# Performance work log

Measured on AMD Instinct MI355X. Metric: run time of the kernel, lower is better.

Reference implementation:

```python
import jax, jax.numpy as jnp
import numpy as np
from jax import lax

WS = 7          # window size
SHIFT = WS // 2 # shift for odd blocks
NH = 4          # num heads
PATCH = 4


def _rel_index(ws):
    # standard Swin relative position index, shape (ws*ws, ws*ws)
    coords = np.stack(np.meshgrid(np.arange(ws), np.arange(ws), indexing='ij')).reshape(2, -1)
    rel = (coords[:, :, None] - coords[:, None, :]).transpose(1, 2, 0)
    rel[..., 0] += ws - 1
    rel[..., 1] += ws - 1
    rel[..., 0] *= 2 * ws - 1
    return jnp.asarray(rel.sum(-1))


def _attn_mask(H, W, ws, s):
    # BasicLayer mask for cyclic shift: (nW, ws*ws, ws*ws) with 0 / -100
    img = np.zeros((H, W))
    cnt = 0
    for hs in (slice(0, -ws), slice(-ws, -s), slice(-s, None)):
        for wsl in (slice(0, -ws), slice(-ws, -s), slice(-s, None)):
            img[hs, wsl] = cnt
            cnt += 1
    mw = img.reshape(H // ws, ws, W // ws, ws).transpose(0, 2, 1, 3).reshape(-1, ws * ws)
    diff = mw[:, None, :] - mw[:, :, None]
    return jnp.asarray(np.where(diff != 0, -100.0, 0.0).astype(np.float32))


def setup_inputs() -> dict:
    key = jax.random.key(0)
    ks = jax.random.split(key, 6)
    C = 128
    return {
        'x': jax.random.normal(ks[0], (16, 3, 448, 448), jnp.float32),
        'conv_w': jax.random.normal(ks[1], (C, 3, PATCH, PATCH), jnp.float32) * 0.02,
        'conv_b': jnp.zeros((C,), jnp.float32),
        'qkv_w': jax.random.normal(ks[2], (2, 3 * C, C), jnp.float32) * 0.02,
        'qkv_b': jnp.zeros((2, 3 * C), jnp.float32),
        'proj_w': jax.random.normal(ks[3], (2, C, C), jnp.float32) * 0.02,
        'proj_b': jnp.zeros((2, C), jnp.float32),
        'rpb': jax.random.normal(ks[4], (2, (2 * WS - 1) ** 2, NH), jnp.float32) * 0.02,
    }


def _forward(x, conv_w, conv_b, qkv_w, qkv_b, proj_w, proj_b, rpb):
    # patch embed: strided conv
    y = lax.conv_general_dilated(x, conv_w, (PATCH, PATCH), 'VALID',
                                 dimension_numbers=('NCHW', 'OIHW', 'NCHW'))
    y = y + conv_b[None, :, None, None]
    B, C, H, W = y.shape
    hd = C // NH
    scale = hd ** -0.5
    N = WS * WS
    nW = (H // WS) * (W // WS)
    t = y.reshape(B, C, H * W).transpose(0, 2, 1)  # (B, L, C)

    rel_idx = _rel_index(WS)                    # (N, N)
    mask = _attn_mask(H, W, WS, SHIFT)          # (nW, N, N)

    for i in range(2):
        shift = 0 if i % 2 == 0 else SHIFT
        xw = t.reshape(B, H, W, C)
        if shift > 0:
            xw = jnp.roll(xw, (-shift, -shift), axis=(1, 2))
        # window partition -> (B*nW, N, C)
        win = xw.reshape(B, H // WS, WS, W // WS, WS, C).transpose(0, 1, 3, 2, 4, 5).reshape(-1, N, C)
        qkv = win @ qkv_w[i].T + qkv_b[i]       # (B*nW, N, 3C)
        qkv = qkv.reshape(-1, N, 3, NH, hd).transpose(2, 0, 3, 1, 4)
        q, k, v = qkv[0], qkv[1], qkv[2]        # (B*nW, NH, N, hd)
        attn = jnp.einsum('wnid,wnjd->wnij', q * scale, k)
        bias = rpb[i][rel_idx].transpose(2, 0, 1)  # (NH, N, N)
        attn = attn + bias[None]
        if shift > 0:
            attn = (attn.reshape(B, nW, NH, N, N) + mask[None, :, None]).reshape(-1, NH, N, N)
        attn = jax.nn.softmax(attn, axis=-1)
        out = jnp.einsum('wnij,wnjd->wnid', attn, v).transpose(0, 2, 1, 3).reshape(-1, N, C)
        out = out @ proj_w[i].T + proj_b[i]
        # window reverse
        xw = out.reshape(B, H // WS, W // WS, WS, WS, C).transpose(0, 1, 3, 2, 4, 5).reshape(B, H, W, C)
        if shift > 0:
            xw = jnp.roll(xw, (shift, shift), axis=(1, 2))
        t = xw.reshape(B, H * W, C)

    return t.reshape(B, H, W, C).transpose(0, 3, 1, 2)  # (B, C, H, W)


def reference(x, conv_w, conv_b, qkv_w, qkv_b, proj_w, proj_b, rpb):
    return _forward(x, conv_w, conv_b, qkv_w, qkv_b, proj_w, proj_b, rpb)
```

## Files before the change

### kernel.cpp

```cpp
#include <hip/hip_runtime.h>

#define BB 16
#define CC 128
#define HH 112
#define NHH 4
#define WSZ 7
#define NN 49
#define SH 3

typedef _Float16 h8 __attribute__((ext_vector_type(8)));
typedef _Float16 h4 __attribute__((ext_vector_type(4)));
typedef float f4 __attribute__((ext_vector_type(4)));

__device__ __forceinline__ int rid3(int p) { return p < 105 ? 0 : (p < 109 ? 1 : 2); }

#define SWZ(row, j, CH) ((row) * ((CH) * 8) + (((((j) >> 3) ^ (row)) & ((CH) - 1)) << 3) + ((j) & 7))

__device__ __forceinline__ h4 pack4(f4 v) {
  h4 r; r[0] = (_Float16)v[0]; r[1] = (_Float16)v[1];
  r[2] = (_Float16)v[2]; r[3] = (_Float16)v[3];
  return r;
}

__global__ __launch_bounds__(256) void conv_embed(const float* __restrict__ x,
    const float* __restrict__ cw, const float* __restrict__ cb, _Float16* __restrict__ t0) {
  __shared__ float xs[3][4][448];
  __shared__ float wT[48][128];
  __shared__ float cbs[128];
  int bid = blockIdx.x;
  int b = bid / HH, oh = bid % HH;
  int tid = threadIdx.x;
  for (int idx = tid; idx < 3 * 4 * 448; idx += 256) {
    int ch = idx / 1792;
    int r = (idx / 448) & 3;
    int col = idx % 448;
    xs[ch][r][col] = x[((b * 3 + ch) * 448 + (oh * 4 + r)) * 448 + col];
  }
  for (int idx = tid; idx < 6144; idx += 256) {
    int c = idx / 48, k = idx - c * 48;
    wT[k][c] = cw[idx];
  }
  if (tid < 128) cbs[tid] = cb[tid];
  __syncthreads();
  int c0 = (tid & 31) << 2;
  int gg = tid >> 5;
  for (int it = 0; it < 4; ++it) {
    int gw0 = it * 32 + gg * 4;
    if (gw0 >= HH) break;
    float acc[4][4] = {};
#pragma unroll
    for (int k = 0; k < 48; ++k) {
      int ch = k >> 4, r = (k >> 2) & 3, j = k & 3;
      float4 wv = *(const float4*)&wT[k][c0];
#pragma unroll
      for (int d = 0; d < 4; ++d) {
        float xv = xs[ch][r][(gw0 + d) * 4 + j];
        acc[d][0] = fmaf(xv, wv.x, acc[d][0]);
        acc[d][1] = fmaf(xv, wv.y, acc[d][1]);
        acc[d][2] = fmaf(xv, wv.z, acc[d][2]);
        acc[d][3] = fmaf(xv, wv.w, acc[d][3]);
      }
    }
    float4 bv = *(const float4*)&cbs[c0];
#pragma unroll
    for (int d = 0; d < 4; ++d) {
      int gw = gw0 + d;
      h4 o;
      o[0] = (_Float16)(acc[d][0] + bv.x); o[1] = (_Float16)(acc[d][1] + bv.y);
      o[2] = (_Float16)(acc[d][2] + bv.z); o[3] = (_Float16)(acc[d][3] + bv.w);
      *(h4*)&t0[((size_t)(b * HH + oh) * HH + gw) * CC + c0] = o;
    }
  }
}

__global__ void prep(const float* __restrict__ qw, const float* __restrict__ qb,
                     const float* __restrict__ pw, const float* __restrict__ rpb,
                     _Float16* __restrict__ qwh, float* __restrict__ qbs,
                     _Float16* __restrict__ pwh, _Float16* __restrict__ biasT) {
  const float scale = 0.17677669529663687f;
  int tid0 = blockIdx.x * blockDim.x + threadIdx.x;
  int stride = gridDim.x * blockDim.x;
  for (int idx = tid0; idx < 2 * 384 * 128; idx += stride) {
    int n = (idx >> 7) % 384;
    float v = qw[idx];
    if (n < 128) v *= scale;
    qwh[idx] = (_Float16)v;
  }
  for (int idx = tid0; idx < 2 * 384; idx += stride) {
    int n = idx % 384;
    float v = qb[idx];
    if (n < 128) v *= scale;
    qbs[idx] = v;
  }
  for (int idx = tid0; idx < 2 * 128 * 128; idx += stride)
    pwh[idx] = (_Float16)pw[idx];
  for (int idx = tid0; idx < 2 * 4 * 4 * 4 * 64 * 4; idx += stride) {
    int r = idx & 3;
    int lane = (idx >> 2) & 63;
    int it = (idx >> 8) & 3;
    int jt = (idx >> 10) & 3;
    int hh = (idx >> 12) & 3;
    int ll = idx >> 14;
    int i = it * 16 + (lane & 15);
    int j = jt * 16 + ((lane >> 4) * 4) + r;
    float v = 0.f;
    if (i < NN && j < NN) {
      int rel = ((i / 7 - j / 7) + 6) * 13 + ((i % 7 - j % 7) + 6);
      v = rpb[(ll * 169 + rel) * NHH + hh];
    }
    biasT[idx] = (_Float16)v;
  }
}

#define RA 0
#define RB 8192
__global__ __launch_bounds__(256, 4) void swin_layer(
    const _Float16* __restrict__ tin, _Float16* __restrict__ toutB, float* __restrict__ outN,
    const _Float16* __restrict__ qwh, const float* __restrict__ qbs,
    const _Float16* __restrict__ pwh, const float* __restrict__ pb,
    const _Float16* __restrict__ biasT, int shift, int writeN) {
  __shared__ _Float16 sm[16384];

  int tid = threadIdx.x;
  int wid = (blockIdx.x & 7) * 512 + (blockIdx.x >> 3);
  int b = wid >> 8;
  int wh = (wid >> 4) & 15, ww = wid & 15;
  int w = tid >> 6, l = tid & 63, li = l & 15, lg = l >> 4;
  int h = w;
  const int hb = RB + h * 2048;

  for (int c = tid; c < 64 * 16; c += 256) {
    int n = c >> 4, k0 = (c & 15) * 8;
    int gh = wh * WSZ + n / 7 + shift; if (gh >= HH) gh -= HH;
    int gw = ww * WSZ + n % 7 + shift; if (gw >= HH) gw -= HH;
    h8 v = *(const h8*)(tin + ((size_t)(b * HH + gh) * HH + gw) * CC + k0);
    *(h8*)&sm[RA + SWZ(n, k0, 16)] = v;
  }
  __syncthreads();

  h8 Kf[4], Qf[4];

  {
    f4 accK[2][4], accQ[2][4];
#pragma unroll
    for (int half = 0; half < 2; ++half) {
      float4 bk = *(const float4*)&qbs[128 + h * 32 + half * 16 + lg * 4];
      float4 bq = *(const float4*)&qbs[h * 32 + half * 16 + lg * 4];
#pragma unroll
      for (int nt = 0; nt < 4; ++nt) {
        accK[half][nt] = f4{bk.x, bk.y, bk.z, bk.w};
        accQ[half][nt] = f4{bq.x, bq.y, bq.z, bq.w};
      }
    }
#pragma unroll
    for (int ks = 0; ks < 4; ++ks) {
      h8 bW[4];
#pragma unroll
      for (int nt = 0; nt < 4; ++nt)
        bW[nt] = *(const h8*)&sm[RA + SWZ(nt * 16 + li, ks * 32 + lg * 8, 16)];
#pragma unroll
      for (int half = 0; half < 2; ++half) {
        h8 aK = *(const h8*)(qwh + (size_t)((8 + 2 * h + half) * 16 + li) * 128 + ks * 32 + lg * 8);
        h8 aQ = *(const h8*)(qwh + (size_t)((2 * h + half) * 16 + li) * 128 + ks * 32 + lg * 8);
#pragma unroll
        for (int nt = 0; nt < 4; ++nt) {
          accK[half][nt] = __builtin_amdgcn_mfma_f32_16x16x32_f16(aK, bW[nt], accK[half][nt], 0, 0, 0);
          accQ[half][nt] = __builtin_amdgcn_mfma_f32_16x16x32_f16(aQ, bW[nt], accQ[half][nt], 0, 0, 0);
        }
      }
    }
#pragma unroll
    for (int half = 0; half < 2; ++half)
#pragma unroll
      for (int nt = 0; nt < 4; ++nt)
        *(h4*)&sm[hb + SWZ(nt * 16 + li, half * 16 + lg * 4, 4)] = pack4(accK[half][nt]);
#pragma unroll
    for (int jt = 0; jt < 4; ++jt)
      Kf[jt] = *(const h8*)&sm[hb + SWZ(jt * 16 + li, lg * 8, 4)];
#pragma unroll
    for (int half = 0; half < 2; ++half)
#pragma unroll
      for (int nt = 0; nt < 4; ++nt)
        *(h4*)&sm[hb + SWZ(nt * 16 + li, half * 16 + lg * 4, 4)] = pack4(accQ[half][nt]);
#pragma unroll
    for (int it = 0; it < 4; ++it)
      Qf[it] = *(const h8*)&sm[hb + SWZ(it * 16 + li, lg * 8, 4)];
  }

  {
    f4 acc[4][2];
#pragma unroll
    for (int ct = 0; ct < 2; ++ct) {
      float bv = qbs[256 + h * 32 + ct * 16 + li];
#pragma unroll
      for (int nt = 0; nt < 4; ++nt) acc[nt][ct] = f4{bv, bv, bv, bv};
    }
#pragma unroll
    for (int ks = 0; ks < 4; ++ks) {
      h8 bW[4];
#pragma unroll
      for (int nt = 0; nt < 4; ++nt)
        bW[nt] = *(const h8*)&sm[RA + SWZ(nt * 16 + li, ks * 32 + lg * 8, 16)];
      h8 wv[2];
#pragma unroll
      for (int ct = 0; ct < 2; ++ct)
        wv[ct] = *(const h8*)(qwh + (size_t)((16 + 2 * h + ct) * 16 + li) * 128 + ks * 32 + lg * 8);
#pragma unroll
      for (int nt = 0; nt < 4; ++nt)
#pragma unroll
        for (int ct = 0; ct < 2; ++ct)
          acc[nt][ct] = __builtin_amdgcn_mfma_f32_16x16x32_f16(bW[nt], wv[ct], acc[nt][ct], 0, 0, 0);
    }
#pragma unroll
    for (int nt = 0; nt < 4; ++nt)
#pragma unroll
      for (int ct = 0; ct < 2; ++ct)
        *(h4*)&sm[hb + SWZ(ct * 16 + li, nt * 16 + lg * 4, 8)] = pack4(acc[nt][ct]);
  }

  float inv[4];
  h4 P4[4][4];
  {
    f4 s[4][4];
    const _Float16* bT = biasT + h * 4096;
#pragma unroll
    for (int jt = 0; jt < 4; ++jt)
#pragma unroll
      for (int it = 0; it < 4; ++it) {
        h4 bb = *(const h4*)&bT[(jt * 4 + it) * 256 + l * 4];
        s[jt][it] = f4{(float)bb[0], (float)bb[1], (float)bb[2], (float)bb[3]};
      }
    __builtin_amdgcn_s_setprio(1);
#pragma unroll
    for (int jt = 0; jt < 4; ++jt)
#pragma unroll
      for (int it = 0; it < 4; ++it)
        s[jt][it] = __builtin_amdgcn_mfma_f32_16x16x32_f16(Kf[jt], Qf[it], s[jt][it], 0, 0, 0);
    __builtin_amdgcn_s_setprio(0);
#pragma unroll
    for (int jt = 0; jt < 4; ++jt)
#pragma unroll
      for (int it = 0; it < 4; ++it)
#pragma unroll
        for (int r = 0; r < 4; ++r) {
          int j = jt * 16 + lg * 4 + r;
          s[jt][it][r] = (j < NN) ? s[jt][it][r] : -1e30f;
        }
    if (shift && (wh == 15 || ww == 15)) {
      int regi[4], regj[4][4];
#pragma unroll
      for (int it = 0; it < 4; ++it) {
        int i = it * 16 + li;
        regi[it] = rid3(wh * WSZ + i / 7) * 3 + rid3(ww * WSZ + i % 7);
      }
#pragma unroll
      for (int jt = 0; jt < 4; ++jt)
#pragma unroll
        for (int r = 0; r < 4; ++r) {
          int j = jt * 16 + lg * 4 + r;
          regj[jt][r] = rid3(wh * WSZ + j / 7) * 3 + rid3(ww * WSZ + j % 7);
        }
#pragma unroll
      for (int jt = 0; jt < 4; ++jt)
#pragma unroll
        for (int it = 0; it < 4; ++it)
#pragma unroll
          for (int r = 0; r < 4; ++r)
            if (regj[jt][r] != regi[it]) s[jt][it][r] -= 100.f;
    }
#pragma unroll
    for (int it = 0; it < 4; ++it) {
      float mx = -1e30f;
#pragma unroll
      for (int jt = 0; jt < 4; ++jt)
#pragma unroll
        for (int r = 0; r < 4; ++r) mx = fmaxf(mx, s[jt][it][r]);
      mx = fmaxf(mx, __shfl_xor(mx, 16));
      mx = fmaxf(mx, __shfl_xor(mx, 32));
      float sum = 0.f;
#pragma unroll
      for (int jt = 0; jt < 4; ++jt)
#pragma unroll
        for (int r = 0; r < 4; ++r) {
          float e = __expf(s[jt][it][r] - mx);
          s[jt][it][r] = e;
          sum += e;
        }
      sum += __shfl_xor(sum, 16);
      sum += __shfl_xor(sum, 32);
      inv[it] = 1.f / sum;
    }
#pragma unroll
    for (int jt = 0; jt < 4; ++jt)
#pragma unroll
      for (int it = 0; it < 4; ++it)
        P4[jt][it] = pack4(s[jt][it]);
  }

  f4 o[2][4] = {};
  {
    h8 aV[2][2];
#pragma unroll
    for (int mt = 0; mt < 2; ++mt)
#pragma unroll
      for (int ks = 0; ks < 2; ++ks)
        aV[mt][ks] = *(const h8*)&sm[hb + SWZ(mt * 16 + li, ks * 32 + lg * 8, 8)];
#pragma unroll
    for (int half = 0; half < 2; ++half) {
#pragma unroll
      for (int jt2 = 0; jt2 < 2; ++jt2)
#pragma unroll
        for (int it = 0; it < 4; ++it)
          *(h4*)&sm[hb + SWZ(it * 16 + li, jt2 * 16 + lg * 4, 4)] = P4[half * 2 + jt2][it];
      h8 bP[4];
#pragma unroll
      for (int nt = 0; nt < 4; ++nt)
        bP[nt] = *(const h8*)&sm[hb + SWZ(nt * 16 + li, lg * 8, 4)];
      __builtin_amdgcn_s_setprio(1);
#pragma unroll
      for (int mt = 0; mt < 2; ++mt)
#pragma unroll
        for (int nt = 0; nt < 4; ++nt)
          o[mt][nt] = __builtin_amdgcn_mfma_f32_16x16x32_f16(aV[mt][half], bP[nt], o[mt][nt], 0, 0, 0);
      __builtin_amdgcn_s_setprio(0);
    }
  }

  h8 pa[2][4];
  float4 pbb[2];
#pragma unroll
  for (int mi = 0; mi < 2; ++mi) {
    pbb[mi] = *(const float4*)&pb[(w * 2 + mi) * 16 + lg * 4];
#pragma unroll
    for (int ks = 0; ks < 4; ++ks)
      pa[mi][ks] = *(const h8*)(pwh + (size_t)((w * 2 + mi) * 16 + li) * 128 + ks * 32 + lg * 8);
  }

#pragma unroll
  for (int mt = 0; mt < 2; ++mt)
#pragma unroll
    for (int nt = 0; nt < 4; ++nt) {
      int i = nt * 16 + li;
      float is = inv[nt];
      h4 v = {(_Float16)(o[mt][nt][0] * is), (_Float16)(o[mt][nt][1] * is),
              (_Float16)(o[mt][nt][2] * is), (_Float16)(o[mt][nt][3] * is)};
      *(h4*)&sm[hb + SWZ(i, mt * 16 + lg * 4, 4)] = v;
    }
  __syncthreads();

  {
    f4 acc[2][4];
#pragma unroll
    for (int mi = 0; mi < 2; ++mi)
#pragma unroll
      for (int nt = 0; nt < 4; ++nt)
        acc[mi][nt] = f4{pbb[mi].x, pbb[mi].y, pbb[mi].z, pbb[mi].w};
    __builtin_amdgcn_s_setprio(1);
#pragma unroll
    for (int ks = 0; ks < 4; ++ks) {
      h8 bO[4];
#pragma unroll
      for (int nt = 0; nt < 4; ++nt)
        bO[nt] = *(const h8*)&sm[RB + ks * 2048 + SWZ(nt * 16 + li, lg * 8, 4)];
#pragma unroll
      for (int mi = 0; mi < 2; ++mi)
#pragma unroll
        for (int nt = 0; nt < 4; ++nt)
          acc[mi][nt] = __builtin_amdgcn_mfma_f32_16x16x32_f16(pa[mi][ks], bO[nt], acc[mi][nt], 0, 0, 0);
    }
    __builtin_amdgcn_s_setprio(0);
    if (!writeN) {
#pragma unroll
      for (int mi = 0; mi < 2; ++mi) {
        int dbase = (w * 2 + mi) * 16 + lg * 4;
#pragma unroll
        for (int nt = 0; nt < 4; ++nt) {
          int i = nt * 16 + li;
          h4 v = {(_Float16)acc[mi][nt][0], (_Float16)acc[mi][nt][1],
                  (_Float16)acc[mi][nt][2], (_Float16)acc[mi][nt][3]};
          *(h4*)&sm[RA + SWZ(i, dbase, 16)] = v;
        }
      }
      __syncthreads();
      for (int cidx = tid; cidx < NN * 16; cidx += 256) {
        int tok = cidx >> 4, c = cidx & 15;
        h8 v = *(const h8*)&sm[RA + SWZ(tok, c * 8, 16)];
        int gh = wh * WSZ + tok / 7;
        int gw = ww * WSZ + tok % 7;
        *(h8*)&toutB[((size_t)(b * HH + gh) * HH + gw) * CC + c * 8] = v;
      }
    } else {
#pragma unroll
      for (int mi = 0; mi < 2; ++mi) {
        int dbase = (w * 2 + mi) * 16 + lg * 4;
#pragma unroll
        for (int nt = 0; nt < 4; ++nt) {
          int i = nt * 16 + li;
          if (i < NN) {
            int gh = wh * WSZ + i / 7 + shift; if (gh >= HH) gh -= HH;
            int gw = ww * WSZ + i % 7 + shift; if (gw >= HH) gw -= HH;
            size_t bse = ((size_t)(b * CC + dbase) * HH + gh) * HH + gw;
            outN[bse] = acc[mi][nt][0];
            outN[bse + (size_t)HH * HH] = acc[mi][nt][1];
            outN[bse + (size_t)2 * HH * HH] = acc[mi][nt][2];
            outN[bse + (size_t)3 * HH * HH] = acc[mi][nt][3];
          }
        }
      }
    }
  }
}

extern "C" void kernel_launch(void* const* d_in, const int* in_sizes, int n_in,
                              void* d_out, int out_size, void* d_ws, size_t ws_size,
                              hipStream_t stream) {
  const float* x = (const float*)d_in[0];
  const float* cw = (const float*)d_in[1];
  const float* cb = (const float*)d_in[2];
  const float* qkvw = (const float*)d_in[3];
  const float* qkvb = (const float*)d_in[4];
  const float* projw = (const float*)d_in[5];
  const float* projb = (const float*)d_in[6];
  const float* rpb = (const float*)d_in[7];
  float* out = (float*)d_out;

  char* ws = (char*)d_ws;
  _Float16* t0 = (_Float16*)ws;
  size_t off = (size_t)BB * HH * HH * CC * 2;
  _Float16* qwh = (_Float16*)(ws + off);  off += 2 * 384 * 128 * 2;
  _Float16* pwh = (_Float16*)(ws + off);  off += 2 * 128 * 128 * 2;
  float* qbs = (float*)(ws + off);        off += 2 * 384 * 4;
  _Float16* biasT = (_Float16*)(ws + off);

  prep<<<224, 256, 0, stream>>>(qkvw, qkvb, projw, rpb, qwh, qbs, pwh, biasT);
  conv_embed<<<BB * HH, 256, 0, stream>>>(x, cw, cb, t0);

  swin_layer<<<4096, 256, 0, stream>>>(t0, t0, nullptr,
      qwh, qbs, pwh, projb, biasT, 0, 0);
  swin_layer<<<4096, 256, 0, stream>>>(t0, nullptr, out,
      qwh + 384 * 128, qbs + 384, pwh + 128 * 128, projb + 128,
      biasT + 16384, SH, 1);
}
```

Before: 260.8 us.

## Process four windows per block with register prefetch of next window

Each block now loops over four consecutive windows instead of one, and the grid shrinks from 4096 to 1024 blocks. The next window's input tokens are loaded into registers during the current window's compute and written to shared memory at the start of the next iteration, overlapping global loads with MFMA work. Weight pointers are pinned in scalar registers with an empty asm so they stay uniform. The change adds register pressure from the prefetch buffer and extra barriers. With fewer blocks, parallelism and tail balance may also suffer.

```diff
diff --git a/kernel.cpp b/kernel.cpp
--- a/kernel.cpp
+++ b/kernel.cpp
@@ -122,288 +122,322 @@
   __shared__ _Float16 sm[16384];
 
   int tid = threadIdx.x;
-  int wid = (blockIdx.x & 7) * 512 + (blockIdx.x >> 3);
-  int b = wid >> 8;
-  int wh = (wid >> 4) & 15, ww = wid & 15;
   int w = tid >> 6, l = tid & 63, li = l & 15, lg = l >> 4;
   int h = w;
   const int hb = RB + h * 2048;
-
-  for (int c = tid; c < 64 * 16; c += 256) {
-    int n = c >> 4, k0 = (c & 15) * 8;
-    int gh = wh * WSZ + n / 7 + shift; if (gh >= HH) gh -= HH;
-    int gw = ww * WSZ + n % 7 + shift; if (gw >= HH) gw -= HH;
-    h8 v = *(const h8*)(tin + ((size_t)(b * HH + gh) * HH + gw) * CC + k0);
-    *(h8*)&sm[RA + SWZ(n, k0, 16)] = v;
-  }
-  __syncthreads();
-
-  h8 Kf[4], Qf[4];
-
-  {
-    f4 accK[2][4], accQ[2][4];
-#pragma unroll
-    for (int half = 0; half < 2; ++half) {
-      float4 bk = *(const float4*)&qbs[128 + h * 32 + half * 16 + lg * 4];
-      float4 bq = *(const float4*)&qbs[h * 32 + half * 16 + lg * 4];
+  int wid0 = (((blockIdx.x & 7) << 7) + (blockIdx.x >> 3)) << 2;
+
+  h8 pf[4];
+
+  for (int itw = 0; itw < 4; ++itw) {
+    int wid = wid0 + itw;
+    int b = wid >> 8;
+    int wh = (wid >> 4) & 15, ww = wid & 15;
+
+    const _Float16* qwp = qwh; const float* qbp = qbs;
+    const _Float16* pwp = pwh; const float* pbp = pb;
+    const _Float16* btp = biasT;
+    asm volatile("" : "+s"(qwp), "+s"(qbp), "+s"(pwp), "+s"(pbp), "+s"(btp));
+
+    if (itw == 0) {
+      for (int c = tid; c < 64 * 16; c += 256) {
+        int n = c >> 4, k0 = (c & 15) * 8;
+        int gh = wh * WSZ + n / 7 + shift; if (gh >= HH) gh -= HH;
+        int gw = ww * WSZ + n % 7 + shift; if (gw >= HH) gw -= HH;
+        h8 v = *(const h8*)(tin + ((size_t)(b * HH + gh) * HH + gw) * CC + k0);
+        *(h8*)&sm[RA + SWZ(n, k0, 16)] = v;
+      }
+    } else {
+      __syncthreads();
+#pragma unroll
+      for (int k = 0; k < 4; ++k) {
+        int c = tid + k * 256;
+        int n = c >> 4, k0 = (c & 15) * 8;
+        *(h8*)&sm[RA + SWZ(n, k0, 16)] = pf[k];
+      }
+    }
+    __syncthreads();
+
+    h8 Kf[4], Qf[4];
+
+    {
+      f4 accK[2][4], accQ[2][4];
+#pragma unroll
+      for (int half = 0; half < 2; ++half) {
+        float4 bk = *(const float4*)&qbp[128 + h * 32 + half * 16 + lg * 4];
+        float4 bq = *(const float4*)&qbp[h * 32 + half * 16 + lg * 4];
+#pragma unroll
+        for (int nt = 0; nt < 4; ++nt) {
+          accK[half][nt] = f4{bk.x, bk.y, bk.z, bk.w};
+          accQ[half][nt] = f4{bq.x, bq.y, bq.z, bq.w};
+        }
+      }
+#pragma unroll
+      for (int ks = 0; ks < 4; ++ks) {
+        h8 bW[4];
+#pragma unroll
+        for (int nt = 0; nt < 4; ++nt)
+          bW[nt] = *(const h8*)&sm[RA + SWZ(nt * 16 + li, ks * 32 + lg * 8, 16)];
+#pragma unroll
+        for (int half = 0; half < 2; ++half) {
+          h8 aK = *(const h8*)(qwp + (size_t)((8 + 2 * h + half) * 16 + li) * 128 + ks * 32 + lg * 8);
+          h8 aQ = *(const h8*)(qwp + (size_t)((2 * h + half) * 16 + li) * 128 + ks * 32 + lg * 8);
+#pragma unroll
+          for (int nt = 0; nt < 4; ++nt) {
+            accK[half][nt] = __builtin_amdgcn_mfma_f32_16x16x32_f16(aK, bW[nt], accK[half][nt], 0, 0, 0);
+            accQ[half][nt] = __builtin_amdgcn_mfma_f32_16x16x32_f16(aQ, bW[nt], accQ[half][nt], 0, 0, 0);
+          }
+        }
+      }
+#pragma unroll
+      for (int half = 0; half < 2; ++half)
+#pragma unroll
+        for (int nt = 0; nt < 4; ++nt)
+          *(h4*)&sm[hb + SWZ(nt * 16 + li, half * 16 + lg * 4, 4)] = pack4(accK[half][nt]);
+#pragma unroll
+      for (int jt = 0; jt < 4; ++jt)
+        Kf[jt] = *(const h8*)&sm[hb + SWZ(jt * 16 + li, lg * 8, 4)];
+#pragma unroll
+      for (int half = 0; half < 2; ++half)
+#pragma unroll
+        for (int nt = 0; nt < 4; ++nt)
+          *(h4*)&sm[hb + SWZ(nt * 16 + li, half * 16 + lg * 4, 4)] = pack4(accQ[half][nt]);
+#pragma unroll
+      for (int it = 0; it < 4; ++it)
+        Qf[it] = *(const h8*)&sm[hb + SWZ(it * 16 + li, lg * 8, 4)];
+    }
+
+    {
+      f4 acc[4][2];
+#pragma unroll
+      for (int ct = 0; ct < 2; ++ct) {
+        float bv = qbp[256 + h * 32 + ct * 16 + li];
+#pragma unroll
+        for (int nt = 0; nt < 4; ++nt) acc[nt][ct] = f4{bv, bv, bv, bv};
+      }
+#pragma unroll
+      for (int ks = 0; ks < 4; ++ks) {
+        h8 bW[4];
+#pragma unroll
+        for (int nt = 0; nt < 4; ++nt)
+          bW[nt] = *(const h8*)&sm[RA + SWZ(nt * 16 + li, ks * 32 + lg * 8, 16)];
+        h8 wv[2];
+#pragma unroll
+        for (int ct = 0; ct < 2; ++ct)
+          wv[ct] = *(const h8*)(qwp + (size_t)((16 + 2 * h + ct) * 16 + li) * 128 + ks * 32 + lg * 8);
+#pragma unroll
+        for (int nt = 0; nt < 4; ++nt)
+#pragma unroll
+          for (int ct = 0; ct < 2; ++ct)
+            acc[nt][ct] = __builtin_amdgcn_mfma_f32_16x16x32_f16(bW[nt], wv[ct], acc[nt][ct], 0, 0, 0);
+      }
+#pragma unroll
+      for (int nt = 0; nt < 4; ++nt)
+#pragma unroll
+        for (int ct = 0; ct < 2; ++ct)
+          *(h4*)&sm[hb + SWZ(ct * 16 + li, nt * 16 + lg * 4, 8)] = pack4(acc[nt][ct]);
+    }
+
+    float inv[4];
+    h4 P4[4][4];
+    {
+      f4 s[4][4];
+      const _Float16* bT = btp + h * 4096;
+#pragma unroll
+      for (int jt = 0; jt < 4; ++jt)
+#pragma unroll
+        for (int it = 0; it < 4; ++it) {
+          h4 bb = *(const h4*)&bT[(jt * 4 + it) * 256 + l * 4];
+          s[jt][it] = f4{(float)bb[0], (float)bb[1], (float)bb[2], (float)bb[3]};
+        }
+      __builtin_amdgcn_s_setprio(1);
+#pragma unroll
+      for (int jt = 0; jt < 4; ++jt)
+#pragma unroll
+        for (int it = 0; it < 4; ++it)
+          s[jt][it] = __builtin_amdgcn_mfma_f32_16x16x32_f16(Kf[jt], Qf[it], s[jt][it], 0, 0, 0);
+      __builtin_amdgcn_s_setprio(0);
+#pragma unroll
+      for (int jt = 0; jt < 4; ++jt)
+#pragma unroll
+        for (int it = 0; it < 4; ++it)
+#pragma unroll
+          for (int r = 0; r < 4; ++r) {
+            int j = jt * 16 + lg * 4 + r;
+            s[jt][it][r] = (j < NN) ? s[jt][it][r] : -1e30f;
+          }
+      if (shift && (wh == 15 || ww == 15)) {
+        int regi[4], regj[4][4];
+#pragma unroll
+        for (int it = 0; it < 4; ++it) {
+          int i = it * 16 + li;
+          regi[it] = rid3(wh * WSZ + i / 7) * 3 + rid3(ww * WSZ + i % 7);
+        }
+#pragma unroll
+        for (int jt = 0; jt < 4; ++jt)
+#pragma unroll
+          for (int r = 0; r < 4; ++r) {
+            int j = jt * 16 + lg * 4 + r;
+            regj[jt][r] = rid3(wh * WSZ + j / 7) * 3 + rid3(ww * WSZ + j % 7);
+          }
+#pragma unroll
+        for (int jt = 0; jt < 4; ++jt)
+#pragma unroll
+          for (int it = 0; it < 4; ++it)
+#pragma unroll
+            for (int r = 0; r < 4; ++r)
+              if (regj[jt][r] != regi[it]) s[jt][it][r] -= 100.f;
+      }
+#pragma unroll
+      for (int it = 0; it < 4; ++it) {
+        float mx = -1e30f;
+#pragma unroll
+        for (int jt = 0; jt < 4; ++jt)
+#pragma unroll
+          for (int r = 0; r < 4; ++r) mx = fmaxf(mx, s[jt][it][r]);
+        mx = fmaxf(mx, __shfl_xor(mx, 16));
+        mx = fmaxf(mx, __shfl_xor(mx, 32));
+        float sum = 0.f;
+#pragma unroll
+        for (int jt = 0; jt < 4; ++jt)
+#pragma unroll
+          for (int r = 0; r < 4; ++r) {
+            float e = __expf(s[jt][it][r] - mx);
+            s[jt][it][r] = e;
+            sum += e;
+          }
+        sum += __shfl_xor(sum, 16);
+        sum += __shfl_xor(sum, 32);
+        inv[it] = 1.f / sum;
+      }
+#pragma unroll
+      for (int jt = 0; jt < 4; ++jt)
+#pragma unroll
+        for (int it = 0; it < 4; ++it)
+          P4[jt][it] = pack4(s[jt][it]);
+    }
+
+    f4 o[2][4] = {};
+    {
+      h8 aV[2][2];
+#pragma unroll
+      for (int mt = 0; mt < 2; ++mt)
+#pragma unroll
+        for (int ks = 0; ks < 2; ++ks)
+          aV[mt][ks] = *(const h8*)&sm[hb + SWZ(mt * 16 + li, ks * 32 + lg * 8, 8)];
+#pragma unroll
+      for (int half = 0; half < 2; ++half) {
+#pragma unroll
+        for (int jt2 = 0; jt2 < 2; ++jt2)
+#pragma unroll
+          for (int it = 0; it < 4; ++it)
+            *(h4*)&sm[hb + SWZ(it * 16 + li, jt2 * 16 + lg * 4, 4)] = P4[half * 2 + jt2][it];
+        h8 bP[4];
+#pragma unroll
+        for (int nt = 0; nt < 4; ++nt)
+          bP[nt] = *(const h8*)&sm[hb + SWZ(nt * 16 + li, lg * 8, 4)];
+        __builtin_amdgcn_s_setprio(1);
+#pragma unroll
+        for (int mt = 0; mt < 2; ++mt)
+#pragma unroll
+          for (int nt = 0; nt < 4; ++nt)
+            o[mt][nt] = __builtin_amdgcn_mfma_f32_16x16x32_f16(aV[mt][half], bP[nt], o[mt][nt], 0, 0, 0);
+        __builtin_amdgcn_s_setprio(0);
+      }
+    }
+
+    if (itw < 3) {
+      int widN = wid + 1;
+      int bN = widN >> 8, whN = (widN >> 4) & 15, wwN = widN & 15;
+#pragma unroll
+      for (int k = 0; k < 4; ++k) {
+        int c = tid + k * 256;
+        int n = c >> 4, k0 = (c & 15) * 8;
+        int gh = whN * WSZ + n / 7 + shift; if (gh >= HH) gh -= HH;
+        int gw = wwN * WSZ + n % 7 + shift; if (gw >= HH) gw -= HH;
+        pf[k] = *(const h8*)(tin + ((size_t)(bN * HH + gh) * HH + gw) * CC + k0);
+      }
+    }
+
+    h8 pa[2][4];
+    float4 pbb[2];
+#pragma unroll
+    for (int mi = 0; mi < 2; ++mi) {
+      pbb[mi] = *(const float4*)&pbp[(w * 2 + mi) * 16 + lg * 4];
+#pragma unroll
+      for (int ks = 0; ks < 4; ++ks)
+        pa[mi][ks] = *(const h8*)(pwp + (size_t)((w * 2 + mi) * 16 + li) * 128 + ks * 32 + lg * 8);
+    }
+
+#pragma unroll
+    for (int mt = 0; mt < 2; ++mt)
 #pragma unroll
       for (int nt = 0; nt < 4; ++nt) {
-        accK[half][nt] = f4{bk.x, bk.y, bk.z, bk.w};
-        accQ[half][nt] = f4{bq.x, bq.y, bq.z, bq.w};
-      }
-    }
-#pragma unroll
-    for (int ks = 0; ks < 4; ++ks) {
-      h8 bW[4];
-#pragma unroll
-      for (int nt = 0; nt < 4; ++nt)
-        bW[nt] = *(const h8*)&sm[RA + SWZ(nt * 16 + li, ks * 32 + lg * 8, 16)];
-#pragma unroll
-      for (int half = 0; half < 2; ++half) {
-        h8 aK = *(const h8*)(qwh + (size_t)((8 + 2 * h + half) * 16 + li) * 128 + ks * 32 + lg * 8);
-        h8 aQ = *(const h8*)(qwh + (size_t)((2 * h + half) * 16 + li) * 128 + ks * 32 + lg * 8);
-#pragma unroll
-        for (int nt = 0; nt < 4; ++nt) {
-          accK[half][nt] = __builtin_amdgcn_mfma_f32_16x16x32_f16(aK, bW[nt], accK[half][nt], 0, 0, 0);
-          accQ[half][nt] = __builtin_amdgcn_mfma_f32_16x16x32_f16(aQ, bW[nt], accQ[half][nt], 0, 0, 0);
-        }
-      }
-    }
-#pragma unroll
-    for (int half = 0; half < 2; ++half)
-#pragma unroll
-      for (int nt = 0; nt < 4; ++nt)
-        *(h4*)&sm[hb + SWZ(nt * 16 + li, half * 16 + lg * 4, 4)] = pack4(accK[half][nt]);
-#pragma unroll
-    for (int jt = 0; jt < 4; ++jt)
-      Kf[jt] = *(const h8*)&sm[hb + SWZ(jt * 16 + li, lg * 8, 4)];
-#pragma unroll
-    for (int half = 0; half < 2; ++half)
-#pragma unroll
-      for (int nt = 0; nt < 4; ++nt)
-        *(h4*)&sm[hb + SWZ(nt * 16 + li, half * 16 + lg * 4, 4)] = pack4(accQ[half][nt]);
-#pragma unroll
-    for (int it = 0; it < 4; ++it)
-      Qf[it] = *(const h8*)&sm[hb + SWZ(it * 16 + li, lg * 8, 4)];
-  }
-
-  {
-    f4 acc[4][2];
-#pragma unroll
-    for (int ct = 0; ct < 2; ++ct) {
-      float bv = qbs[256 + h * 32 + ct * 16 + li];
-#pragma unroll
-      for (int nt = 0; nt < 4; ++nt) acc[nt][ct] = f4{bv, bv, bv, bv};
-    }
-#pragma unroll
-    for (int ks = 0; ks < 4; ++ks) {
-      h8 bW[4];
-#pragma unroll
-      for (int nt = 0; nt < 4; ++nt)
-        bW[nt] = *(const h8*)&sm[RA + SWZ(nt * 16 + li, ks * 32 + lg * 8, 16)];
-      h8 wv[2];
-#pragma unroll
-      for (int ct = 0; ct < 2; ++ct)
-        wv[ct] = *(const h8*)(qwh + (size_t)((16 + 2 * h + ct) * 16 + li) * 128 + ks * 32 + lg * 8);
-#pragma unroll
-      for (int nt = 0; nt < 4; ++nt)
-#pragma unroll
-        for (int ct = 0; ct < 2; ++ct)
-          acc[nt][ct] = __builtin_amdgcn_mfma_f32_16x16x32_f16(bW[nt], wv[ct], acc[nt][ct], 0, 0, 0);
-    }
-#pragma unroll
-    for (int nt = 0; nt < 4; ++nt)
-#pragma unroll
-      for (int ct = 0; ct < 2; ++ct)
-        *(h4*)&sm[hb + SWZ(ct * 16 + li, nt * 16 + lg * 4, 8)] = pack4(acc[nt][ct]);
-  }
-
-  float inv[4];
-  h4 P4[4][4];
-  {
-    f4 s[4][4];
-    const _Float16* bT = biasT + h * 4096;
-#pragma unroll
-    for (int jt = 0; jt < 4; ++jt)
-#pragma unroll
-      for (int it = 0; it < 4; ++it) {
-        h4 bb = *(const h4*)&bT[(jt * 4 + it) * 256 + l * 4];
-        s[jt][it] = f4{(float)bb[0], (float)bb[1], (float)bb[2], (float)bb[3]};
-      }
-    __builtin_amdgcn_s_setprio(1);
-#pragma unroll
-    for (int jt = 0; jt < 4; ++jt)
-#pragma unroll
-      for (int it = 0; it < 4; ++it)
-        s[jt][it] = __builtin_amdgcn_mfma_f32_16x16x32_f16(Kf[jt], Qf[it], s[jt][it], 0, 0, 0);
-    __builtin_amdgcn_s_setprio(0);
-#pragma unroll
-    for (int jt = 0; jt < 4; ++jt)
-#pragma unroll
-      for (int it = 0; it < 4; ++it)
-#pragma unroll
-        for (int r = 0; r < 4; ++r) {
-          int j = jt * 16 + lg * 4 + r;
-          s[jt][it][r] = (j < NN) ? s[jt][it][r] : -1e30f;
-        }
-    if (shift && (wh == 15 || ww == 15)) {
-      int regi[4], regj[4][4];
-#pragma unroll
-      for (int it = 0; it < 4; ++it) {
-        int i = it * 16 + li;
-        regi[it] = rid3(wh * WSZ + i / 7) * 3 + rid3(ww * WSZ + i % 7);
-      }
-#pragma unroll
-      for (int jt = 0; jt < 4; ++jt)
-#pragma unroll
-        for (int r = 0; r < 4; ++r) {
-          int j = jt * 16 + lg * 4 + r;
-          regj[jt][r] = rid3(wh * WSZ + j / 7) * 3 + rid3(ww * WSZ + j % 7);
-        }
-#pragma unroll
-      for (int jt = 0; jt < 4; ++jt)
-#pragma unroll
-        for (int it = 0; it < 4; ++it)
-#pragma unroll
-          for (int r = 0; r < 4; ++r)
-            if (regj[jt][r] != regi[it]) s[jt][it][r] -= 100.f;
-    }
-#pragma unroll
-    for (int it = 0; it < 4; ++it) {
-      float mx = -1e30f;
-#pragma unroll
-      for (int jt = 0; jt < 4; ++jt)
-#pragma unroll
-        for (int r = 0; r < 4; ++r) mx = fmaxf(mx, s[jt][it][r]);
-      mx = fmaxf(mx, __shfl_xor(mx, 16));
-      mx = fmaxf(mx, __shfl_xor(mx, 32));
-      float sum = 0.f;
-#pragma unroll
-      for (int jt = 0; jt < 4; ++jt)
-#pragma unroll
-        for (int r = 0; r < 4; ++r) {
-          float e = __expf(s[jt][it][r] - mx);
-          s[jt][it][r] = e;
-          sum += e;
-        }
-      sum += __shfl_xor(sum, 16);
-      sum += __shfl_xor(sum, 32);
-      inv[it] = 1.f / sum;
-    }
-#pragma unroll
-    for (int jt = 0; jt < 4; ++jt)
-#pragma unroll
-      for (int it = 0; it < 4; ++it)
-        P4[jt][it] = pack4(s[jt][it]);
-  }
-
-  f4 o[2][4] = {};
-  {
-    h8 aV[2][2];
-#pragma unroll
-    for (int mt = 0; mt < 2; ++mt)
-#pragma unroll
-      for (int ks = 0; ks < 2; ++ks)
-        aV[mt][ks] = *(const h8*)&sm[hb + SWZ(mt * 16 + li, ks * 32 + lg * 8, 8)];
-#pragma unroll
-    for (int half = 0; half < 2; ++half) {
-#pragma unroll
-      for (int jt2 = 0; jt2 < 2; ++jt2)
-#pragma unroll
-        for (int it = 0; it < 4; ++it)
-          *(h4*)&sm[hb + SWZ(it * 16 + li, jt2 * 16 + lg * 4, 4)] = P4[half * 2 + jt2][it];
-      h8 bP[4];
-#pragma unroll
-      for (int nt = 0; nt < 4; ++nt)
-        bP[nt] = *(const h8*)&sm[hb + SWZ(nt * 16 + li, lg * 8, 4)];
+        int i = nt * 16 + li;
+        float is = inv[nt];
+        h4 v = {(_Float16)(o[mt][nt][0] * is), (_Float16)(o[mt][nt][1] * is),
+                (_Float16)(o[mt][nt][2] * is), (_Float16)(o[mt][nt][3] * is)};
+        *(h4*)&sm[hb + SWZ(i, mt * 16 + lg * 4, 4)] = v;
+      }
+    __syncthreads();
+
+    {
+      f4 acc[2][4];
+#pragma unroll
+      for (int mi = 0; mi < 2; ++mi)
+#pragma unroll
+        for (int nt = 0; nt < 4; ++nt)
+          acc[mi][nt] = f4{pbb[mi].x, pbb[mi].y, pbb[mi].z, pbb[mi].w};
       __builtin_amdgcn_s_setprio(1);
 #pragma unroll
-      for (int mt = 0; mt < 2; ++mt)
-#pragma unroll
-        for (int nt = 0; nt < 4; ++nt)
-          o[mt][nt] = __builtin_amdgcn_mfma_f32_16x16x32_f16(aV[mt][half], bP[nt], o[mt][nt], 0, 0, 0);
+      for (int ks = 0; ks < 4; ++ks) {
+        h8 bO[4];
+#pragma unroll
+        for (int nt = 0; nt < 4; ++nt)
+          bO[nt] = *(const h8*)&sm[RB + ks * 2048 + SWZ(nt * 16 + li, lg * 8, 4)];
+#pragma unroll
+        for (int mi = 0; mi < 2; ++mi)
+#pragma unroll
+          for (int nt = 0; nt < 4; ++nt)
+            acc[mi][nt] = __builtin_amdgcn_mfma_f32_16x16x32_f16(pa[mi][ks], bO[nt], acc[mi][nt], 0, 0, 0);
+      }
       __builtin_amdgcn_s_setprio(0);
-    }
-  }
-
-  h8 pa[2][4];
-  float4 pbb[2];
-#pragma unroll
-  for (int mi = 0; mi < 2; ++mi) {
-    pbb[mi] = *(const float4*)&pb[(w * 2 + mi) * 16 + lg * 4];
-#pragma unroll
-    for (int ks = 0; ks < 4; ++ks)
-      pa[mi][ks] = *(const h8*)(pwh + (size_t)((w * 2 + mi) * 16 + li) * 128 + ks * 32 + lg * 8);
-  }
-
-#pragma unroll
-  for (int mt = 0; mt < 2; ++mt)
-#pragma unroll
-    for (int nt = 0; nt < 4; ++nt) {
-      int i = nt * 16 + li;
-      float is = inv[nt];
-      h4 v = {(_Float16)(o[mt][nt][0] * is), (_Float16)(o[mt][nt][1] * is),
-              (_Float16)(o[mt][nt][2] * is), (_Float16)(o[mt][nt][3] * is)};
-      *(h4*)&sm[hb + SWZ(i, mt * 16 + lg * 4, 4)] = v;
-    }
-  __syncthreads();
-
-  {
-    f4 acc[2][4];
-#pragma unroll
-    for (int mi = 0; mi < 2; ++mi)
-#pragma unroll
-      for (int nt = 0; nt < 4; ++nt)
-        acc[mi][nt] = f4{pbb[mi].x, pbb[mi].y, pbb[mi].z, pbb[mi].w};
-    __builtin_amdgcn_s_setprio(1);
-#pragma unroll
-    for (int ks = 0; ks < 4; ++ks) {
-      h8 bO[4];
-#pragma unroll
-      for (int nt = 0; nt < 4; ++nt)
-        bO[nt] = *(const h8*)&sm[RB + ks * 2048 + SWZ(nt * 16 + li, lg * 8, 4)];
-#pragma unroll
-      for (int mi = 0; mi < 2; ++mi)
-#pragma unroll
-        for (int nt = 0; nt < 4; ++nt)
-          acc[mi][nt] = __builtin_amdgcn_mfma_f32_16x16x32_f16(pa[mi][ks], bO[nt], acc[mi][nt], 0, 0, 0);
-    }
-    __builtin_amdgcn_s_setprio(0);
-    if (!writeN) {
-#pragma unroll
-      for (int mi = 0; mi < 2; ++mi) {
-        int dbase = (w * 2 + mi) * 16 + lg * 4;
-#pragma unroll
-        for (int nt = 0; nt < 4; ++nt) {
-          int i = nt * 16 + li;
-          h4 v = {(_Float16)acc[mi][nt][0], (_Float16)acc[mi][nt][1],
-                  (_Float16)acc[mi][nt][2], (_Float16)acc[mi][nt][3]};
-          *(h4*)&sm[RA + SWZ(i, dbase, 16)] = v;
-        }
-      }
-      __syncthreads();
-      for (int cidx = tid; cidx < NN * 16; cidx += 256) {
-        int tok = cidx >> 4, c = cidx & 15;
-        h8 v = *(const h8*)&sm[RA + SWZ(tok, c * 8, 16)];
-        int gh = wh * WSZ + tok / 7;
-        int gw = ww * WSZ + tok % 7;
-        *(h8*)&toutB[((size_t)(b * HH + gh) * HH + gw) * CC + c * 8] = v;
-      }
-    } else {
-#pragma unroll
-      for (int mi = 0; mi < 2; ++mi) {
-        int dbase = (w * 2 + mi) * 16 + lg * 4;
-#pragma unroll
-        for (int nt = 0; nt < 4; ++nt) {
-          int i = nt * 16 + li;
-          if (i < NN) {
-            int gh = wh * WSZ + i / 7 + shift; if (gh >= HH) gh -= HH;
-            int gw = ww * WSZ + i % 7 + shift; if (gw >= HH) gw -= HH;
-            size_t bse = ((size_t)(b * CC + dbase) * HH + gh) * HH + gw;
-            outN[bse] = acc[mi][nt][0];
-            outN[bse + (size_t)HH * HH] = acc[mi][nt][1];
-            outN[bse + (size_t)2 * HH * HH] = acc[mi][nt][2];
-            outN[bse + (size_t)3 * HH * HH] = acc[mi][nt][3];
+      if (!writeN) {
+#pragma unroll
+        for (int mi = 0; mi < 2; ++mi) {
+          int dbase = (w * 2 + mi) * 16 + lg * 4;
+#pragma unroll
+          for (int nt = 0; nt < 4; ++nt) {
+            int i = nt * 16 + li;
+            h4 v = {(_Float16)acc[mi][nt][0], (_Float16)acc[mi][nt][1],
+                    (_Float16)acc[mi][nt][2], (_Float16)acc[mi][nt][3]};
+            *(h4*)&sm[RA + SWZ(i, dbase, 16)] = v;
+          }
+        }
+        __syncthreads();
+        for (int cidx = tid; cidx < NN * 16; cidx += 256) {
+          int tok = cidx >> 4, c = cidx & 15;
+          h8 v = *(const h8*)&sm[RA + SWZ(tok, c * 8, 16)];
+          int gh = wh * WSZ + tok / 7;
+          int gw = ww * WSZ + tok % 7;
+          *(h8*)&toutB[((size_t)(b * HH + gh) * HH + gw) * CC + c * 8] = v;
+        }
+      } else {
+#pragma unroll
+        for (int mi = 0; mi < 2; ++mi) {
+          int dbase = (w * 2 + mi) * 16 + lg * 4;
+#pragma unroll
+          for (int nt = 0; nt < 4; ++nt) {
+            int i = nt * 16 + li;
+            if (i < NN) {
+              int gh = wh * WSZ + i / 7 + shift; if (gh >= HH) gh -= HH;
+              int gw = ww * WSZ + i % 7 + shift; if (gw >= HH) gw -= HH;
+              size_t bse = ((size_t)(b * CC + dbase) * HH + gh) * HH + gw;
+              outN[bse] = acc[mi][nt][0];
+              outN[bse + (size_t)HH * HH] = acc[mi][nt][1];
+              outN[bse + (size_t)2 * HH * HH] = acc[mi][nt][2];
+              outN[bse + (size_t)3 * HH * HH] = acc[mi][nt][3];
+            }
           }
         }
       }
@@ -435,9 +469,9 @@
   prep<<<224, 256, 0, stream>>>(qkvw, qkvb, projw, rpb, qwh, qbs, pwh, biasT);
   conv_embed<<<BB * HH, 256, 0, stream>>>(x, cw, cb, t0);
 
-  swin_layer<<<4096, 256, 0, stream>>>(t0, t0, nullptr,
+  swin_layer<<<1024, 256, 0, stream>>>(t0, t0, nullptr,
       qwh, qbs, pwh, projb, biasT, 0, 0);
-  swin_layer<<<4096, 256, 0, stream>>>(t0, nullptr, out,
+  swin_layer<<<1024, 256, 0, stream>>>(t0, nullptr, out,
       qwh + 384 * 128, qbs + 384, pwh + 128 * 128, projb + 128,
       biasT + 16384, SH, 1);
 }
```

After: 437.6 us. 1.68x slower.
